# Kernel optimization log

Hardware: AMD Instinct MI355X
Metric: run time of the kernel (lower is better)

Reference implementation:

```python
import jax, jax.numpy as jnp
import numpy as np

N_RULE, N_TOKEN = 256, 32000
F_IN, F_ACT, H = 512, 512, 1024  # input_feature_size, action_feature_size, output_feature_size
L, B = 128, 64


def setup_inputs() -> dict:
    key = jax.random.key(0)
    ks = jax.random.split(key, 8)
    s_ih = 1.0 / np.sqrt(H)
    return {
        "input_feature": jax.random.normal(ks[0], (B, F_IN), dtype=jnp.float32),
        "previous_actions": jax.random.randint(ks[1], (L, B, 3), 0, N_RULE, dtype=jnp.int64),
        "mask": jnp.ones((L, B), dtype=jnp.float32),
        "hidden_state": jnp.zeros((B, H), dtype=jnp.float32),
        "state": jnp.zeros((B, H), dtype=jnp.float32),
        "rule_embed": jax.random.normal(ks[2], (N_RULE, F_ACT), dtype=jnp.float32),
        "token_embed": jax.random.normal(ks[3], (N_TOKEN, F_ACT), dtype=jnp.float32),
        "W_ih": jax.random.uniform(ks[4], (4 * H, F_IN + F_ACT), jnp.float32, -s_ih, s_ih),
        "W_hh": jax.random.uniform(ks[5], (4 * H, H), jnp.float32, -s_ih, s_ih),
        "b_ih": jax.random.uniform(ks[6], (4 * H,), jnp.float32, -s_ih, s_ih),
        "b_hh": jax.random.uniform(ks[7], (4 * H,), jnp.float32, -s_ih, s_ih),
    }


def _masked_embed(table, idx):
    # EmbeddingWithMask: index == -1 maps to the zero vector
    valid = (idx != -1)
    emb = table[jnp.where(valid, idx, 0)]
    return emb * valid[..., None].astype(table.dtype)


def reference(input_feature, previous_actions, mask, hidden_state, state,
              rule_embed, token_embed, W_ih, W_hh, b_ih, b_hh):
    prev_rules = previous_actions[..., 0]   # (L, B)
    prev_tokens = previous_actions[..., 1]  # (L, B)
    act = _masked_embed(rule_embed, prev_rules) + _masked_embed(token_embed, prev_tokens)  # (L,B,F_ACT)

    # Per-step input is concat([input_feature, act_t]); precompute the whole
    # input projection x @ W_ih^T + biases once (big batched GEMM).
    l, b = act.shape[0], act.shape[1]
    Wx, Wa = W_ih[:, :input_feature.shape[1]], W_ih[:, input_feature.shape[1]:]
    xg = (input_feature @ Wx.T)[None] + jnp.einsum('lba,ga->lbg', act, Wa) + (b_ih + b_hh)  # (L,B,4H)

    def step(carry, xg_t):
        h, c = carry
        g = xg_t + h @ W_hh.T                     # (B, 4H)
        i, f, gg, o = jnp.split(g, 4, axis=-1)    # torch LSTMCell gate order
        i, f, o = jax.nn.sigmoid(i), jax.nn.sigmoid(f), jax.nn.sigmoid(o)
        c1 = f * c + i * jnp.tanh(gg)
        h1 = o * jnp.tanh(c1)
        return (h1, c1), h1

    (h_n, c_n), hs = jax.lax.scan(step, (hidden_state, state), xg)
    return hs, h_n, c_n
```

## Files before the change

### kernel.cpp

```cpp
#include <hip/hip_runtime.h>
#include <hip/hip_bf16.h>

typedef __attribute__((ext_vector_type(8))) short bf16x8;
typedef __attribute__((ext_vector_type(4))) float f32x4;

#define L_SEQ 128
#define BATCH 64
#define HID   1024
#define GATES 4096
#define NWG   256
#define UPW   4
#define FSTR  4

__device__ inline short f2bf_s(float f) {
  __hip_bfloat16 h = __float2bfloat16(f);
  union { __hip_bfloat16 hh; short s; } u; u.hh = h; return u.s;
}
__device__ inline float sigm(float x) { return 1.f / (1.f + __expf(-x)); }
__device__ inline float tanh_f(float x) {
  x = fminf(x, 15.f);
  float e = __expf(2.f * x);
  return (e - 1.f) / (e + 1.f);
}

__global__ void k_init(const float* __restrict__ hidden, const float* __restrict__ x,
                       const float* __restrict__ bih, const float* __restrict__ bhh,
                       __hip_bfloat16* __restrict__ h_all0, __hip_bfloat16* __restrict__ x_bf,
                       float* __restrict__ bias2, unsigned* __restrict__ bar) {
  int gid = blockIdx.x * 256 + threadIdx.x;
  if (gid < BATCH * HID) h_all0[gid] = __float2bfloat16(hidden[gid]);
  if (gid < BATCH * 512) x_bf[gid]  = __float2bfloat16(x[gid]);
  if (gid < GATES)       bias2[gid] = bih[gid] + bhh[gid];
  if (gid < 16384)       bar[gid] = 0u;
}

__global__ void k_wsplit(const float* __restrict__ Wih,
                         __hip_bfloat16* __restrict__ Wx, __hip_bfloat16* __restrict__ Wa) {
  int e = blockIdx.x * 256 + threadIdx.x;
  int g = e >> 7;
  int ko = (e & 127) << 3;
  const float* src = Wih + (size_t)g * 1024 + ko;
  float4 f0 = *(const float4*)(src);
  float4 f1 = *(const float4*)(src + 4);
  union { bf16x8 v; short s[8]; } o;
  o.s[0]=f2bf_s(f0.x); o.s[1]=f2bf_s(f0.y); o.s[2]=f2bf_s(f0.z); o.s[3]=f2bf_s(f0.w);
  o.s[4]=f2bf_s(f1.x); o.s[5]=f2bf_s(f1.y); o.s[6]=f2bf_s(f1.z); o.s[7]=f2bf_s(f1.w);
  if (ko < 512) *(bf16x8*)(Wx + (size_t)g * 512 + ko)        = o.v;
  else          *(bf16x8*)(Wa + (size_t)g * 512 + (ko - 512)) = o.v;
}

__global__ void k_act(const int* __restrict__ pa, const float* __restrict__ remb,
                      const float* __restrict__ temb, __hip_bfloat16* __restrict__ act) {
  int row = blockIdx.x;
  int tid = threadIdx.x;
  int r  = pa[row * 3 + 0];
  int tk = pa[row * 3 + 1];
  float sr = (r  != -1) ? 1.f : 0.f; int ri = (r  != -1) ? r  : 0;
  float st = (tk != -1) ? 1.f : 0.f; int ti = (tk != -1) ? tk : 0;
  const float4* rr = (const float4*)(remb + (size_t)ri * 512);
  const float4* tr = (const float4*)(temb + (size_t)ti * 512);
  float4 a = rr[tid * 2], b4 = rr[tid * 2 + 1];
  float4 c4 = tr[tid * 2], d4 = tr[tid * 2 + 1];
  union { bf16x8 v; short s[8]; } o;
  o.s[0]=f2bf_s(sr*a.x + st*c4.x);  o.s[1]=f2bf_s(sr*a.y + st*c4.y);
  o.s[2]=f2bf_s(sr*a.z + st*c4.z);  o.s[3]=f2bf_s(sr*a.w + st*c4.w);
  o.s[4]=f2bf_s(sr*b4.x + st*d4.x); o.s[5]=f2bf_s(sr*b4.y + st*d4.y);
  o.s[6]=f2bf_s(sr*b4.z + st*d4.z); o.s[7]=f2bf_s(sr*b4.w + st*d4.w);
  *(bf16x8*)(act + (size_t)row * 512 + tid * 8) = o.v;
}

template<int MODE>
__global__ __launch_bounds__(256) void k_gemm(
    const __hip_bfloat16* __restrict__ A, const __hip_bfloat16* __restrict__ B,
    const float* __restrict__ addend, float* __restrict__ Cf,
    __hip_bfloat16* __restrict__ Cb, int M) {
  __shared__ __hip_bfloat16 At[128][72];
  __shared__ __hip_bfloat16 Bt[128][72];
  const int tid = threadIdx.x;
  const int m0 = blockIdx.y * 128, n0 = blockIdx.x * 128;
  const int w = tid >> 6, lane = tid & 63;
  const int wm = (w >> 1) * 64, wn = (w & 1) * 64;
  const int lm = lane & 15, quad = lane >> 4;
  const int srow = tid >> 1, shalf = (tid & 1) * 32;
  f32x4 acc[4][4] = {};
  for (int k0 = 0; k0 < 512; k0 += 64) {
    int arow = m0 + srow;
    if (MODE == 0 && arow >= M) arow = M - 1;
    const bf16x8* ag = (const bf16x8*)(A + (size_t)arow * 512 + k0 + shalf);
    const bf16x8* bg = (const bf16x8*)(B + (size_t)(n0 + srow) * 512 + k0 + shalf);
    bf16x8 av[4], bv[4];
#pragma unroll
    for (int q = 0; q < 4; ++q) { av[q] = ag[q]; bv[q] = bg[q]; }
    __syncthreads();
#pragma unroll
    for (int q = 0; q < 4; ++q) {
      *(bf16x8*)(&At[srow][shalf + q * 8]) = av[q];
      *(bf16x8*)(&Bt[srow][shalf + q * 8]) = bv[q];
    }
    __syncthreads();
#pragma unroll
    for (int ks = 0; ks < 2; ++ks) {
      bf16x8 af[4], bf[4];
#pragma unroll
      for (int i = 0; i < 4; ++i) {
        af[i] = *(const bf16x8*)(&At[wm + i * 16 + lm][ks * 32 + quad * 8]);
        bf[i] = *(const bf16x8*)(&Bt[wn + i * 16 + lm][ks * 32 + quad * 8]);
      }
#pragma unroll
      for (int i = 0; i < 4; ++i)
#pragma unroll
        for (int j = 0; j < 4; ++j)
          acc[i][j] = __builtin_amdgcn_mfma_f32_16x16x32_bf16(af[i], bf[j], acc[i][j], 0, 0, 0);
    }
  }
#pragma unroll
  for (int i = 0; i < 4; ++i) {
    int mrow = m0 + wm + i * 16 + quad * 4;
#pragma unroll
    for (int j = 0; j < 4; ++j) {
      int ncol = n0 + wn + j * 16 + lm;
#pragma unroll
      for (int r = 0; r < 4; ++r) {
        int m = mrow + r;
        if (MODE == 0) {
          if (m < M) Cf[(size_t)m * GATES + ncol] = acc[i][j][r] + addend[ncol];
        } else {
          float v = acc[i][j][r] + addend[(size_t)(m & 63) * GATES + ncol];
          Cb[(size_t)m * GATES + ncol] = __float2bfloat16(v);
        }
      }
    }
  }
}

__global__ __launch_bounds__(256, 1) void k_scan(
    const float* __restrict__ Whh, const __hip_bfloat16* __restrict__ xg,
    const float* __restrict__ state_in, __hip_bfloat16* __restrict__ h_all,
    float* __restrict__ out_hs, float* __restrict__ out_hn, float* __restrict__ out_cn,
    unsigned* __restrict__ bar) {
  __shared__ __hip_bfloat16 Wl[16 * 1024];
  __shared__ float gl[64 * 17];
  __shared__ unsigned long long hpack[BATCH];
  const int tid = threadIdx.x;
  const int wg = blockIdx.x;
  const int u0 = wg * UPW;
  for (int e = tid; e < 16 * 128; e += 256) {
    int j = e >> 7;
    int ko = (e & 127) << 3;
    int gate = j >> 2, uu = j & 3;
    const float* src = Whh + (size_t)(gate * HID + u0 + uu) * HID + ko;
    float4 f0 = *(const float4*)(src);
    float4 f1 = *(const float4*)(src + 4);
    union { bf16x8 v; short s[8]; } o;
    o.s[0]=f2bf_s(f0.x); o.s[1]=f2bf_s(f0.y); o.s[2]=f2bf_s(f0.z); o.s[3]=f2bf_s(f0.w);
    o.s[4]=f2bf_s(f1.x); o.s[5]=f2bf_s(f1.y); o.s[6]=f2bf_s(f1.z); o.s[7]=f2bf_s(f1.w);
    int kq = ko >> 5, qd = (ko >> 3) & 3;
    *(bf16x8*)(&Wl[kq * 512 + j * 32 + qd * 8]) = o.v;
  }
  const int b = tid >> 2, u = tid & 3;
  float c = state_in[b * HID + u0 + u];
  const int w = tid >> 6, lane = tid & 63;
  const int lm = lane & 15, quad = lane >> 4;
  const int m0 = w * 16;
  unsigned* flags = bar;
  const __hip_bfloat16* Wb = Wl + lm * 32 + quad * 8;
  const __hip_bfloat16* xgp0 = xg + (size_t)b * GATES + u0 + u;
  float xi  = __bfloat162float(xgp0[0]);
  float xf  = __bfloat162float(xgp0[1024]);
  float xgg = __bfloat162float(xgp0[2048]);
  float xo  = __bfloat162float(xgp0[3072]);
  unsigned dep = 0;
  __syncthreads();
  for (int t = 0; t < L_SEQ; ++t) {
    const __hip_bfloat16* hsrc = h_all + ((size_t)t + dep) * (BATCH * HID);
    const bf16x8* arow = (const bf16x8*)(hsrc + (m0 + lm) * HID + quad * 8);
    bf16x8 areg[32];
#pragma unroll
    for (int kq = 0; kq < 32; ++kq) areg[kq] = arow[kq * 4];
    __builtin_amdgcn_sched_barrier(0);
    f32x4 acc0 = {0.f, 0.f, 0.f, 0.f}, acc1 = {0.f, 0.f, 0.f, 0.f};
#pragma unroll
    for (int kq = 0; kq < 32; kq += 2) {
      acc0 = __builtin_amdgcn_mfma_f32_16x16x32_bf16(
          areg[kq], *(const bf16x8*)(Wb + (size_t)kq * 512), acc0, 0, 0, 0);
      acc1 = __builtin_amdgcn_mfma_f32_16x16x32_bf16(
          areg[kq + 1], *(const bf16x8*)(Wb + (size_t)(kq + 1) * 512), acc1, 0, 0, 0);
    }
    f32x4 accs = acc0 + acc1;
#pragma unroll
    for (int r = 0; r < 4; ++r) gl[(m0 + quad * 4 + r) * 17 + lm] = accs[r];
    __syncthreads();
    float gi = gl[b * 17 + u]      + xi;
    float gf = gl[b * 17 + 4 + u]  + xf;
    float gg = gl[b * 17 + 8 + u]  + xgg;
    float go = gl[b * 17 + 12 + u] + xo;
    float iv = sigm(gi), fv = sigm(gf), ov = sigm(go), gv = tanh_f(gg);
    c = fv * c + iv * gv;
    float h = ov * tanh_f(c);
    if (t == L_SEQ - 1) {
      __builtin_nontemporal_store(h, &out_hs[((size_t)t * BATCH + b) * HID + u0 + u]);
      __builtin_nontemporal_store(h, &out_hn[(size_t)b * HID + u0 + u]);
      __builtin_nontemporal_store(c, &out_cn[(size_t)b * HID + u0 + u]);
    } else {
      ((unsigned short*)hpack)[b * 4 + u] = (unsigned short)f2bf_s(h);
      __syncthreads();
      unsigned long long* hdst64 =
          (unsigned long long*)(h_all + ((size_t)(t + 1)) * (BATCH * HID));
      if (tid < BATCH) {
        __hip_atomic_store(&hdst64[(tid * HID + u0) >> 2], hpack[tid],
                           __ATOMIC_RELAXED, __HIP_MEMORY_SCOPE_SYSTEM);
      }
      unsigned target = (unsigned)(t + 1);
      __builtin_amdgcn_s_waitcnt(0);
      if (tid == 0)
        __hip_atomic_store(&flags[wg * FSTR], target, __ATOMIC_RELAXED,
                           __HIP_MEMORY_SCOPE_SYSTEM);
      __builtin_amdgcn_sched_barrier(0);
      __builtin_nontemporal_store(h, &out_hs[((size_t)t * BATCH + b) * HID + u0 + u]);
      const __hip_bfloat16* xgp = xg + ((size_t)(t + 1) * BATCH + b) * GATES + u0 + u;
      float nxi  = __bfloat162float(xgp[0]);
      float nxf  = __bfloat162float(xgp[1024]);
      float nxgg = __bfloat162float(xgp[2048]);
      float nxo  = __bfloat162float(xgp[3072]);
      unsigned v;
      for (;;) {
        v = __hip_atomic_load(&flags[tid * FSTR], __ATOMIC_RELAXED,
                              __HIP_MEMORY_SCOPE_SYSTEM);
        if (v >= target) break;
        __builtin_amdgcn_s_sleep(1);
      }
      dep = v >> 20;
      __syncthreads();
      xi = nxi; xf = nxf; xgg = nxgg; xo = nxo;
    }
  }
}

extern "C" void kernel_launch(void* const* d_in, const int* in_sizes, int n_in,
                              void* d_out, int out_size, void* d_ws, size_t ws_size,
                              hipStream_t stream) {
  const float* x      = (const float*)d_in[0];
  const int*   pa     = (const int*)d_in[1];
  const float* hidden = (const float*)d_in[3];
  const float* state  = (const float*)d_in[4];
  const float* remb   = (const float*)d_in[5];
  const float* temb   = (const float*)d_in[6];
  const float* Wih    = (const float*)d_in[7];
  const float* Whh    = (const float*)d_in[8];
  const float* bih    = (const float*)d_in[9];
  const float* bhh    = (const float*)d_in[10];

  char* ws = (char*)d_ws;
  size_t off = 0;
  auto take = [&](size_t bytes) { char* p = ws + off; off += (bytes + 255) & ~(size_t)255; return p; };
  unsigned* bar         = (unsigned*)take(16384 * 4);
  __hip_bfloat16* h_all = (__hip_bfloat16*)take((size_t)L_SEQ * BATCH * HID * 2);
  __hip_bfloat16* x_bf  = (__hip_bfloat16*)take((size_t)BATCH * 512 * 2);
  float* bias2          = (float*)take((size_t)GATES * 4);
  __hip_bfloat16* Wx    = (__hip_bfloat16*)take((size_t)GATES * 512 * 2);
  __hip_bfloat16* Wa    = (__hip_bfloat16*)take((size_t)GATES * 512 * 2);
  __hip_bfloat16* act   = (__hip_bfloat16*)take((size_t)8192 * 512 * 2);
  float* y0             = (float*)take((size_t)BATCH * GATES * 4);
  __hip_bfloat16* xg    = (__hip_bfloat16*)take((size_t)8192 * GATES * 2);

  float* out_hs = (float*)d_out;
  float* out_hn = out_hs + (size_t)L_SEQ * BATCH * HID;
  float* out_cn = out_hn + (size_t)BATCH * HID;

  hipLaunchKernelGGL(k_init, dim3(256), dim3(256), 0, stream, hidden, x, bih, bhh, h_all, x_bf, bias2, bar);
  hipLaunchKernelGGL(k_wsplit, dim3(2048), dim3(256), 0, stream, Wih, Wx, Wa);
  hipLaunchKernelGGL(k_act, dim3(8192), dim3(64), 0, stream, pa, remb, temb, act);
  hipLaunchKernelGGL((k_gemm<0>), dim3(32, 1), dim3(256), 0, stream,
                     x_bf, Wx, bias2, y0, (__hip_bfloat16*)nullptr, 64);
  hipLaunchKernelGGL((k_gemm<1>), dim3(32, 64), dim3(256), 0, stream,
                     act, Wa, y0, (float*)nullptr, xg, 8192);
  void* args[] = { (void*)&Whh, (void*)&xg, (void*)&state, (void*)&h_all,
                   (void*)&out_hs, (void*)&out_hn, (void*)&out_cn, (void*)&bar };
  (void)hipLaunchCooperativeKernel((void*)k_scan, dim3(NWG), dim3(256), args, 0, stream);
}
```

Before: 1.146 ms.

## Store hidden state in per-workgroup blocked layout and pack flags densely

Rearranges the bf16 hidden-state buffer so each workgroup's 4 units for all 64 batch rows occupy one contiguous 512-byte chunk. The per-step publish is then a contiguous write, and the MFMA A-operand loads are rewritten as pairs of 8-byte reads over the new layout. Barrier flags lose their 4-word stride and become dense, the MFMA chain is split across four accumulators, and the h buffer gains one extra slot. The intent is to cut scattered write traffic and polling cost in the latency-bound recurrent loop, at the cost of narrower A-fragment loads and possible false sharing on the packed flags.

```diff
diff --git a/kernel.cpp b/kernel.cpp
--- a/kernel.cpp
+++ b/kernel.cpp
@@ -10,7 +10,7 @@
 #define GATES 4096
 #define NWG   256
 #define UPW   4
-#define FSTR  4
+#define SLOTB (BATCH * HID * 2)
 
 __device__ inline short f2bf_s(float f) {
   __hip_bfloat16 h = __float2bfloat16(f);
@@ -28,7 +28,10 @@
                        __hip_bfloat16* __restrict__ h_all0, __hip_bfloat16* __restrict__ x_bf,
                        float* __restrict__ bias2, unsigned* __restrict__ bar) {
   int gid = blockIdx.x * 256 + threadIdx.x;
-  if (gid < BATCH * HID) h_all0[gid] = __float2bfloat16(hidden[gid]);
+  if (gid < BATCH * HID) {
+    int b = gid >> 10, u = gid & 1023;
+    h_all0[(u >> 2) * 256 + b * 4 + (u & 3)] = __float2bfloat16(hidden[gid]);
+  }
   if (gid < BATCH * 512) x_bf[gid]  = __float2bfloat16(x[gid]);
   if (gid < GATES)       bias2[gid] = bih[gid] + bhh[gid];
   if (gid < 16384)       bar[gid] = 0u;
@@ -172,21 +175,30 @@
   unsigned dep = 0;
   __syncthreads();
   for (int t = 0; t < L_SEQ; ++t) {
-    const __hip_bfloat16* hsrc = h_all + ((size_t)t + dep) * (BATCH * HID);
-    const bf16x8* arow = (const bf16x8*)(hsrc + (m0 + lm) * HID + quad * 8);
-    bf16x8 areg[32];
-#pragma unroll
-    for (int kq = 0; kq < 32; ++kq) areg[kq] = arow[kq * 4];
+    const char* slot = (const char*)h_all + ((size_t)t + dep) * SLOTB;
+    const char* lanebase = slot + (size_t)quad * 1024 + (size_t)(m0 + lm) * 8;
+    union BF8 { bf16x8 v; unsigned long long q[2]; };
+    BF8 areg[32];
+#pragma unroll
+    for (int kq = 0; kq < 32; ++kq) {
+      areg[kq].q[0] = *(const unsigned long long*)(lanebase + (size_t)kq * 4096);
+      areg[kq].q[1] = *(const unsigned long long*)(lanebase + (size_t)kq * 4096 + 512);
+    }
     __builtin_amdgcn_sched_barrier(0);
-    f32x4 acc0 = {0.f, 0.f, 0.f, 0.f}, acc1 = {0.f, 0.f, 0.f, 0.f};
-#pragma unroll
-    for (int kq = 0; kq < 32; kq += 2) {
+    f32x4 acc0 = {0.f,0.f,0.f,0.f}, acc1 = {0.f,0.f,0.f,0.f};
+    f32x4 acc2 = {0.f,0.f,0.f,0.f}, acc3 = {0.f,0.f,0.f,0.f};
+#pragma unroll
+    for (int kq = 0; kq < 32; kq += 4) {
       acc0 = __builtin_amdgcn_mfma_f32_16x16x32_bf16(
-          areg[kq], *(const bf16x8*)(Wb + (size_t)kq * 512), acc0, 0, 0, 0);
+          areg[kq].v,     *(const bf16x8*)(Wb + (size_t)kq * 512),       acc0, 0, 0, 0);
       acc1 = __builtin_amdgcn_mfma_f32_16x16x32_bf16(
-          areg[kq + 1], *(const bf16x8*)(Wb + (size_t)(kq + 1) * 512), acc1, 0, 0, 0);
-    }
-    f32x4 accs = acc0 + acc1;
+          areg[kq + 1].v, *(const bf16x8*)(Wb + (size_t)(kq + 1) * 512), acc1, 0, 0, 0);
+      acc2 = __builtin_amdgcn_mfma_f32_16x16x32_bf16(
+          areg[kq + 2].v, *(const bf16x8*)(Wb + (size_t)(kq + 2) * 512), acc2, 0, 0, 0);
+      acc3 = __builtin_amdgcn_mfma_f32_16x16x32_bf16(
+          areg[kq + 3].v, *(const bf16x8*)(Wb + (size_t)(kq + 3) * 512), acc3, 0, 0, 0);
+    }
+    f32x4 accs = (acc0 + acc1) + (acc2 + acc3);
 #pragma unroll
     for (int r = 0; r < 4; ++r) gl[(m0 + quad * 4 + r) * 17 + lm] = accs[r];
     __syncthreads();
@@ -204,16 +216,16 @@
     } else {
       ((unsigned short*)hpack)[b * 4 + u] = (unsigned short)f2bf_s(h);
       __syncthreads();
-      unsigned long long* hdst64 =
-          (unsigned long long*)(h_all + ((size_t)(t + 1)) * (BATCH * HID));
+      unsigned long long* hdst = (unsigned long long*)
+          ((char*)h_all + (size_t)(t + 1) * SLOTB + (size_t)wg * 512);
       if (tid < BATCH) {
-        __hip_atomic_store(&hdst64[(tid * HID + u0) >> 2], hpack[tid],
+        __hip_atomic_store(&hdst[tid], hpack[tid],
                            __ATOMIC_RELAXED, __HIP_MEMORY_SCOPE_SYSTEM);
       }
       unsigned target = (unsigned)(t + 1);
       __builtin_amdgcn_s_waitcnt(0);
       if (tid == 0)
-        __hip_atomic_store(&flags[wg * FSTR], target, __ATOMIC_RELAXED,
+        __hip_atomic_store(&flags[wg], target, __ATOMIC_RELAXED,
                            __HIP_MEMORY_SCOPE_SYSTEM);
       __builtin_amdgcn_sched_barrier(0);
       __builtin_nontemporal_store(h, &out_hs[((size_t)t * BATCH + b) * HID + u0 + u]);
@@ -224,7 +236,7 @@
       float nxo  = __bfloat162float(xgp[3072]);
       unsigned v;
       for (;;) {
-        v = __hip_atomic_load(&flags[tid * FSTR], __ATOMIC_RELAXED,
+        v = __hip_atomic_load(&flags[tid], __ATOMIC_RELAXED,
                               __HIP_MEMORY_SCOPE_SYSTEM);
         if (v >= target) break;
         __builtin_amdgcn_s_sleep(1);
@@ -254,7 +266,7 @@
   size_t off = 0;
   auto take = [&](size_t bytes) { char* p = ws + off; off += (bytes + 255) & ~(size_t)255; return p; };
   unsigned* bar         = (unsigned*)take(16384 * 4);
-  __hip_bfloat16* h_all = (__hip_bfloat16*)take((size_t)L_SEQ * BATCH * HID * 2);
+  __hip_bfloat16* h_all = (__hip_bfloat16*)take((size_t)(L_SEQ + 1) * BATCH * HID * 2);
   __hip_bfloat16* x_bf  = (__hip_bfloat16*)take((size_t)BATCH * 512 * 2);
   float* bias2          = (float*)take((size_t)GATES * 4);
   __hip_bfloat16* Wx    = (__hip_bfloat16*)take((size_t)GATES * 512 * 2);
```

New measurement: 1.162 ms. About the same (+1.4%).
